# Kernel optimization log

Hardware: AMD Instinct MI355X
Metric: run time of the kernel (lower is better)

The kernel has to match this reference:

```python
import jax
jax.config.update("jax_enable_x64", True)
import jax.numpy as jnp
import numpy as np

SIGMA_2 = 0.1  # SNR = 10 dB -> sigma^2 = 1/10^(10/10)
P = 1.0        # total transmit power

NT, NR, DK, KU, BR = 64, 4, 2, 8, 16
BATCH = 256


def setup_inputs() -> dict:
    key = jax.random.key(0)
    k1, k2 = jax.random.split(key)
    channel = jax.random.normal(k1, (BATCH, NT * NR * BR * 2 * KU), dtype=jnp.float32)
    pred_w = 2 * NR * DK * KU * BR + DK * DK * KU * BR  # 2560
    prediction = jax.random.normal(k2, (BATCH, pred_w), dtype=jnp.float32)
    return {"channel": channel, "prediction": prediction,
            "Nt": NT, "Nr": NR, "dk": DK, "K": KU, "B": BR}


def reference(channel, prediction, Nt, Nr, dk, K, B):
    # --- unpack complex channel: [b, Nt, Nr, B, 2K] -> [b, Nr, Nt, B, K] complex
    Hc = channel.reshape(-1, Nt, Nr, B, 2 * K).astype(jnp.complex128)
    H = Hc[..., :K] + 1j * Hc[..., K:]
    H = jnp.transpose(H, (0, 2, 1, 3, 4))  # [b, Nr, Nt, B, K]

    nu = 2 * Nr * dk * K * B
    u_flat = prediction[:, :nu]
    w_flat = prediction[:, nu:nu + dk * dk * K * B]
    Uc = u_flat.reshape(-1, Nr, dk, B, 2 * K).astype(jnp.complex128)
    U = Uc[..., :K] + 1j * Uc[..., K:]           # [b, Nr, dk, B, K]
    W = w_flat.reshape(-1, dk, dk, B, K).astype(jnp.complex128)  # real-valued W

    # HHU[b,:,:,f,k] = H^H U  -> [b, Nt, dk, B, K]
    HHU = jnp.einsum('brtfk,brdfk->btdfk', jnp.conj(H), U)

    # sum over (rb, user) of sigma2/p * trace(U W U^H)
    tr_UWU = (SIGMA_2 / P) * jnp.einsum('brdfk,bdefk,brefk->b', U, W, jnp.conj(U))
    # sum over (rb, user) of (H^H U) W (H^H U)^H  -> [b, Nt, Nt]
    quad = jnp.einsum('btdfk,bdefk,bsefk->bts', HHU, W, jnp.conj(HHU))
    temp_B = quad + tr_UWU[:, None, None] * jnp.eye(Nt, dtype=jnp.complex128)
    temp_B_inv = jnp.linalg.inv(temp_B)  # batched Nt x Nt complex inverse

    # HUW[b,:,:,k] = sum_rb (H^H U) W  -> [b, Nt, dk, K]
    HUW = jnp.einsum('btdfk,bdefk->btek', HHU, W)
    V0 = jnp.einsum('bts,bsdk->btdk', temp_B_inv, HUW)  # [b, Nt, dk, K]

    # l2-normalize flattened precoder per sample (tf.linalg.normalize)
    flat = V0.reshape(-1, Nt * dk * K)
    flat = flat / jnp.linalg.norm(flat, axis=1, keepdims=True)
    V0 = flat.reshape(-1, Nt, dk, K)

    # power normalization: trace(sum_k V_k V_k^H)
    trace_VV = jnp.einsum('btdk,btdk->b', V0, jnp.conj(V0))
    scale = jnp.sqrt(P / jnp.real(trace_VV).astype(jnp.float32))
    V = V0 * scale.astype(jnp.complex128)[:, None, None, None]

    V = V.reshape(-1, Nt, dk, K, 1)
    return jnp.concatenate([jnp.real(V), jnp.imag(V)], axis=4).astype(jnp.float32)
```

## Files before the change

kernel.cpp:

```cpp
#include <hip/hip_runtime.h>
#include <math.h>


#define SAUG 84
#define STP  65

typedef float v2f __attribute__((ext_vector_type(2)));

namespace {
union alignas(16) ShU {
    struct { float4 TtP[2][2][8][STP]; float4 HtP[2][2][8][STP]; } p1;
    float2 Aug[64][SAUG];
};
union alignas(16) ShV {
    struct { float2 U[4 * 258]; float W[512]; } in;
    float2 xout[64][17];
};
}

__device__ __forceinline__ float2 cmul(float2 x, float2 y) {
    return make_float2(x.x * y.x - x.y * y.y, x.x * y.y + x.y * y.x);
}
__device__ __forceinline__ v2f s2(float s) { return (v2f){s, s}; }

__global__ __launch_bounds__(512, 1)
void uw2v_kernel(const float* __restrict__ channel,
                 const float* __restrict__ prediction,
                 float2* __restrict__ out)
{
    __shared__ ShU sh;
    __shared__ ShV sv;
    __shared__ alignas(16) float2 pivR[2][8][80];
    __shared__ float2 pivI[2][8];
    __shared__ float2 redbuf[8];
    __shared__ float  fred[8];

    const int b   = blockIdx.x;
    const int tid = threadIdx.x;
    const int wv  = tid >> 6;
    const float* pred = prediction + (size_t)b * 2560;
    const float* chan = channel + (size_t)b * 65536;

    #pragma unroll
    for (int i = 0; i < 2; ++i) {
        int m = tid + i * 512;
        int r = m >> 8, d = (m >> 7) & 1, f = (m >> 3) & 15, k = m & 7;
        const float* src = pred + (((r * 2 + d) * 16 + f) << 4);
        sv.in.U[r * 258 + ((d * 16 + f) << 3) + k] = make_float2(src[k], src[k + 8]);
    }
    sv.in.W[tid] = pred[2048 + tid];
    __syncthreads();

    const int half = tid >> 8;
    const int lt   = tid & 255;
    const int t4 = lt >> 2, r4 = lt & 3;
    const int a  = lt >> 4, bb = lt & 15;
    const int bit0 = r4 & 1, bit1 = (r4 >> 1) & 1;
    const int kkb  = 4 * bit0 + 2 * bit1;
    const int mpb  = kkb >> 1;
    const int fbase = half << 3;
    const int tr_r = lt >> 5, tr_d = (lt >> 4) & 1, tr_e = (lt >> 3) & 1, tr_k = lt & 7;

    v2f accA[4][4], accB[4][4];
    #pragma unroll
    for (int i = 0; i < 4; ++i)
        #pragma unroll
        for (int j = 0; j < 4; ++j) {
            accA[i][j] = (v2f){0.f, 0.f};
            accB[i][j] = (v2f){0.f, 0.f};
        }
    float2 huw[4] = {make_float2(0,0), make_float2(0,0), make_float2(0,0), make_float2(0,0)};
    float2 tracc  = make_float2(0.f, 0.f);

    const float* hbase = chan + ((t4 * 4 + r4) << 8) + (fbase << 4);

    #pragma unroll 1
    for (int fi = 0; fi < 8; ++fi) {
        const int f = fbase + fi;
        const float4 ca = *(const float4*)(hbase + (fi << 4) + 0);
        const float4 cb = *(const float4*)(hbase + (fi << 4) + 4);
        const float4 ci = *(const float4*)(hbase + (fi << 4) + 8);
        const float4 cd = *(const float4*)(hbase + (fi << 4) + 12);

        const float4* U0p = (const float4*)&sv.in.U[r4 * 258 + (f << 3)];
        const float4* U1p = (const float4*)&sv.in.U[r4 * 258 + ((16 + f) << 3)];
        const float4 u0q0 = U0p[0], u0q1 = U0p[1], u0q2 = U0p[2], u0q3 = U0p[3];
        const float4 u1q0 = U1p[0], u1q1 = U1p[1], u1q2 = U1p[2], u1q3 = U1p[3];

        float2 val0[8], val1[8];
        #define MK2(K, HR, HI, U0R, U0I, U1R, U1I) \
            val0[K] = make_float2((HR)*(U0R) + (HI)*(U0I), (HR)*(U0I) - (HI)*(U0R)); \
            val1[K] = make_float2((HR)*(U1R) + (HI)*(U1I), (HR)*(U1I) - (HI)*(U1R));
        MK2(0, ca.x, ci.x, u0q0.x, u0q0.y, u1q0.x, u1q0.y)
        MK2(1, ca.y, ci.y, u0q0.z, u0q0.w, u1q0.z, u1q0.w)
        MK2(2, ca.z, ci.z, u0q1.x, u0q1.y, u1q1.x, u1q1.y)
        MK2(3, ca.w, ci.w, u0q1.z, u0q1.w, u1q1.z, u1q1.w)
        MK2(4, cb.x, cd.x, u0q2.x, u0q2.y, u1q2.x, u1q2.y)
        MK2(5, cb.y, cd.y, u0q2.z, u0q2.w, u1q2.z, u1q2.w)
        MK2(6, cb.z, cd.z, u0q3.x, u0q3.y, u1q3.x, u1q3.y)
        MK2(7, cb.w, cd.w, u0q3.z, u0q3.w, u1q3.z, u1q3.w)
        #undef MK2

        float2 s1d0[4], s1d1[4];
        #pragma unroll
        for (int q = 0; q < 4; ++q) {
            float2 k0 = bit0 ? val0[4 + q] : val0[q];
            float2 n0 = bit0 ? val0[q]     : val0[4 + q];
            float2 k1 = bit0 ? val1[4 + q] : val1[q];
            float2 n1 = bit0 ? val1[q]     : val1[4 + q];
            n0.x = __shfl_xor(n0.x, 1); n0.y = __shfl_xor(n0.y, 1);
            n1.x = __shfl_xor(n1.x, 1); n1.y = __shfl_xor(n1.y, 1);
            s1d0[q] = make_float2(k0.x + n0.x, k0.y + n0.y);
            s1d1[q] = make_float2(k1.x + n1.x, k1.y + n1.y);
        }
        float2 h0[2], h1[2];
        #pragma unroll
        for (int jj = 0; jj < 2; ++jj) {
            float2 k0 = bit1 ? s1d0[2 + jj] : s1d0[jj];
            float2 n0 = bit1 ? s1d0[jj]     : s1d0[2 + jj];
            float2 k1 = bit1 ? s1d1[2 + jj] : s1d1[jj];
            float2 n1 = bit1 ? s1d1[jj]     : s1d1[2 + jj];
            n0.x = __shfl_xor(n0.x, 2); n0.y = __shfl_xor(n0.y, 2);
            n1.x = __shfl_xor(n1.x, 2); n1.y = __shfl_xor(n1.y, 2);
            h0[jj] = make_float2(k0.x + n0.x, k0.y + n0.y);
            h1[jj] = make_float2(k1.x + n1.x, k1.y + n1.y);
        }

        if (lt < 128) {
            float w   = sv.in.W[((tr_d * 2 + tr_e) * 16 + f) * 8 + tr_k];
            float2 u1 = sv.in.U[tr_r * 258 + ((tr_d * 16 + f) << 3) + tr_k];
            float2 u2 = sv.in.U[tr_r * 258 + ((tr_e * 16 + f) << 3) + tr_k];
            tracc.x += w * (u1.x * u2.x + u1.y * u2.y);
            tracc.y += w * (u1.y * u2.x - u1.x * u2.y);
        }

        const int p = fi & 1;
        #pragma unroll
        for (int e = 0; e < 2; ++e) {
            float w0a = sv.in.W[(e * 16 + f) * 8 + kkb];
            float w0b = sv.in.W[(e * 16 + f) * 8 + kkb + 1];
            float w1a = sv.in.W[((2 + e) * 16 + f) * 8 + kkb];
            float w1b = sv.in.W[((2 + e) * 16 + f) * 8 + kkb + 1];
            float2 tva = make_float2(h0[0].x * w0a + h1[0].x * w1a,
                                     h0[0].y * w0a + h1[0].y * w1a);
            float2 tvb = make_float2(h0[1].x * w0b + h1[1].x * w1b,
                                     h0[1].y * w0b + h1[1].y * w1b);
            sh.p1.TtP[p][half][e * 4 + mpb][t4] = make_float4(tva.x, tva.y, tvb.x, tvb.y);
            huw[e * 2 + 0].x += tva.x; huw[e * 2 + 0].y += tva.y;
            huw[e * 2 + 1].x += tvb.x; huw[e * 2 + 1].y += tvb.y;
        }
        sh.p1.HtP[p][half][mpb][t4]     = make_float4(h0[0].x, h0[0].y, h0[1].x, h0[1].y);
        sh.p1.HtP[p][half][4 + mpb][t4] = make_float4(h1[0].x, h1[0].y, h1[1].x, h1[1].y);
        __syncthreads();

        #pragma unroll
        for (int mp = 0; mp < 8; ++mp) {
            float4 tq[4], hq[4];
            #pragma unroll
            for (int i = 0; i < 4; ++i) tq[i] = sh.p1.TtP[p][half][mp][a + 16 * i];
            #pragma unroll
            for (int j = 0; j < 4; ++j) hq[j] = sh.p1.HtP[p][half][mp][bb + 16 * j];
            #pragma unroll
            for (int i = 0; i < 4; ++i)
                #pragma unroll
                for (int j = 0; j < 4; ++j) {
                    v2f hq01 = (v2f){hq[j].x, hq[j].y};
                    v2f hq23 = (v2f){hq[j].z, hq[j].w};
                    v2f va = accA[i][j], vb = accB[i][j];
                    va = __builtin_elementwise_fma(s2(tq[i].x), hq01, va);
                    va = __builtin_elementwise_fma(s2(tq[i].z), hq23, va);
                    vb = __builtin_elementwise_fma(s2(tq[i].y), hq01, vb);
                    vb = __builtin_elementwise_fma(s2(tq[i].w), hq23, vb);
                    accA[i][j] = va; accB[i][j] = vb;
                }
        }
    }

    #pragma unroll
    for (int off = 32; off; off >>= 1) {
        tracc.x += __shfl_xor(tracc.x, off);
        tracc.y += __shfl_xor(tracc.y, off);
    }
    if ((tid & 63) == 0) redbuf[wv] = tracc;
    __syncthreads();
    float2 trv = make_float2(0.f, 0.f);
    #pragma unroll
    for (int w = 0; w < 8; ++w) { trv.x += redbuf[w].x; trv.y += redbuf[w].y; }
    trv.x *= 0.1f; trv.y *= 0.1f;

    if (half == 0) {
        #pragma unroll
        for (int i = 0; i < 4; ++i)
            #pragma unroll
            for (int j = 0; j < 4; ++j) {
                float2 v = make_float2(accA[i][j].x + accB[i][j].y,
                                       accB[i][j].x - accA[i][j].y);
                int row = a + 16 * i, col = bb + 16 * j;
                if (row == col) { v.x += trv.x; v.y += trv.y; }
                sh.Aug[row][col] = v;
            }
        #pragma unroll
        for (int e = 0; e < 2; ++e)
            #pragma unroll
            for (int jj = 0; jj < 2; ++jj)
                sh.Aug[t4][64 + e * 8 + kkb + jj] = huw[e * 2 + jj];
    }
    __syncthreads();
    if (half == 1) {
        #pragma unroll
        for (int i = 0; i < 4; ++i)
            #pragma unroll
            for (int j = 0; j < 4; ++j) {
                int row = a + 16 * i, col = bb + 16 * j;
                float2 v = sh.Aug[row][col];
                v.x += accA[i][j].x + accB[i][j].y;
                v.y += accB[i][j].x - accA[i][j].y;
                sh.Aug[row][col] = v;
            }
        #pragma unroll
        for (int e = 0; e < 2; ++e)
            #pragma unroll
            for (int jj = 0; jj < 2; ++jj) {
                int col = 64 + e * 8 + kkb + jj;
                float2 v = sh.Aug[t4][col];
                v.x += huw[e * 2 + jj].x; v.y += huw[e * 2 + jj].y;
                sh.Aug[t4][col] = v;
            }
    }
    __syncthreads();

    const int gi = tid >> 3, gc = tid & 7;
    const int cb = 10 * gc;
    const int lanebase = (tid & 63) & 56;

    v2f xr[10];
    {
        const float4* rp = (const float4*)&sh.Aug[gi][cb];
        float4 q0 = rp[0], q1 = rp[1], q2 = rp[2], q3 = rp[3], q4 = rp[4];
        xr[0] = (v2f){q0.x, q0.y}; xr[1] = (v2f){q0.z, q0.w};
        xr[2] = (v2f){q1.x, q1.y}; xr[3] = (v2f){q1.z, q1.w};
        xr[4] = (v2f){q2.x, q2.y}; xr[5] = (v2f){q2.z, q2.w};
        xr[6] = (v2f){q3.x, q3.y}; xr[7] = (v2f){q3.z, q3.w};
        xr[8] = (v2f){q4.x, q4.y}; xr[9] = (v2f){q4.z, q4.w};
    }

    float2 myipv = make_float2(0.f, 0.f);

    auto rowupd = [](v2f* xr10, const v2f* pr10, float2 L) {
        v2f nLx = s2(-L.x);
        v2f Lyp = (v2f){L.y, -L.y};
        #pragma unroll
        for (int c = 0; c < 10; ++c) {
            v2f prv = pr10[c];
            v2f prsw = (v2f){prv.y, prv.x};
            xr10[c] = __builtin_elementwise_fma(
                nLx, prv, __builtin_elementwise_fma(Lyp, prsw, xr10[c]));
        }
    };

    auto cascade = [&](int chunk, int nb) {
        #pragma unroll
        for (int p = 0; p < 8; ++p) {
            const int col = 8 * chunk + p;
            const int cs  = col / 10;
            float2 cand = make_float2(0.f, 0.f);
            #pragma unroll
            for (int c = 0; c < 10; ++c)
                if (cb + c == col) cand = make_float2(xr[c].x, xr[c].y);
            float2 z, Lv;
            z.x  = __shfl(cand.x, p * 8 + cs);
            z.y  = __shfl(cand.y, p * 8 + cs);
            Lv.x = __shfl(cand.x, lanebase + cs);
            Lv.y = __shfl(cand.y, lanebase + cs);
            float  zi  = 1.0f / (z.x * z.x + z.y * z.y);
            float2 ipv = make_float2(z.x * zi, -z.y * zi);
            const bool isPiv = (gi == col);
            if (isPiv) myipv = ipv;
            v2f pr[10];
            #pragma unroll
            for (int c = 0; c < 10; ++c) {
                pr[c].x = __shfl(xr[c].x, p * 8 + gc);
                pr[c].y = __shfl(xr[c].y, p * 8 + gc);
            }
            if (!isPiv) {
                float2 L = cmul(Lv, ipv);
                rowupd(xr, pr, L);
            }
        }
        const int prw = gi & 7;
        float4* wp = (float4*)&pivR[nb][prw][cb];
        wp[0] = make_float4(xr[0].x, xr[0].y, xr[1].x, xr[1].y);
        wp[1] = make_float4(xr[2].x, xr[2].y, xr[3].x, xr[3].y);
        wp[2] = make_float4(xr[4].x, xr[4].y, xr[5].x, xr[5].y);
        wp[3] = make_float4(xr[6].x, xr[6].y, xr[7].x, xr[7].y);
        wp[4] = make_float4(xr[8].x, xr[8].y, xr[9].x, xr[9].y);
        if (gc == 0) pivI[nb][prw] = myipv;
    };

    auto eliminate = [&](int chunk, int bf) {
        #pragma unroll
        for (int p = 0; p < 8; ++p) {
            const int col = 8 * chunk + p;
            float2 cand = make_float2(0.f, 0.f);
            #pragma unroll
            for (int c = 0; c < 10; ++c)
                if (cb + c == col) cand = make_float2(xr[c].x, xr[c].y);
            float2 Lv;
            Lv.x = __shfl(cand.x, lanebase + col / 10);
            Lv.y = __shfl(cand.y, lanebase + col / 10);
            float2 ipv = pivI[bf][p];
            float2 L = cmul(Lv, ipv);
            const float4* pp = (const float4*)&pivR[bf][p][cb];
            float4 p0 = pp[0], p1 = pp[1], p2 = pp[2], p3 = pp[3], p4 = pp[4];
            v2f pr[10];
            pr[0] = (v2f){p0.x, p0.y}; pr[1] = (v2f){p0.z, p0.w};
            pr[2] = (v2f){p1.x, p1.y}; pr[3] = (v2f){p1.z, p1.w};
            pr[4] = (v2f){p2.x, p2.y}; pr[5] = (v2f){p2.z, p2.w};
            pr[6] = (v2f){p3.x, p3.y}; pr[7] = (v2f){p3.z, p3.w};
            pr[8] = (v2f){p4.x, p4.y}; pr[9] = (v2f){p4.z, p4.w};
            rowupd(xr, pr, L);
        }
    };

    int cur = 0;
    if (wv == 0) cascade(0, 0);
    __syncthreads();

    #pragma unroll 1
    for (int c = 0; c < 8; ++c) {
        if (wv != c) {
            eliminate(c, cur);
            if (wv == c + 1) cascade(c + 1, cur ^ 1);
        }
        __syncthreads();
        cur ^= 1;
    }

    float ss = 0.f;
    if (gc == 6) {
        #pragma unroll
        for (int c = 4; c < 10; ++c) {
            float2 xv = cmul(make_float2(xr[c].x, xr[c].y), myipv);
            ss += xv.x * xv.x + xv.y * xv.y;
            sv.xout[gi][c - 4] = xv;
        }
    } else if (gc == 7) {
        #pragma unroll
        for (int c = 0; c < 10; ++c) {
            float2 xv = cmul(make_float2(xr[c].x, xr[c].y), myipv);
            ss += xv.x * xv.x + xv.y * xv.y;
            sv.xout[gi][6 + c] = xv;
        }
    }
    #pragma unroll
    for (int off = 32; off; off >>= 1) ss += __shfl_xor(ss, off);
    if ((tid & 63) == 0) fred[wv] = ss;
    __syncthreads();
    float total = 0.f;
    #pragma unroll
    for (int w = 0; w < 8; ++w) total += fred[w];
    float invn = rsqrtf(total);
    #pragma unroll
    for (int q = 0; q < 2; ++q) {
        int m = tid + q * 512;
        float2 v = sv.xout[m >> 4][m & 15];
        out[(size_t)b * 1024 + m] = make_float2(v.x * invn, v.y * invn);
    }
}

extern "C" void kernel_launch(void* const* d_in, const int* in_sizes, int n_in,
                              void* d_out, int out_size, void* d_ws, size_t ws_size,
                              hipStream_t stream) {
    const float* channel    = (const float*)d_in[0];
    const float* prediction = (const float*)d_in[1];
    int batch = in_sizes[0] / 65536;
    uw2v_kernel<<<dim3(batch), dim3(512), 0, stream>>>(channel, prediction,
                                                       (float2*)d_out);
}
```

Baseline: 155.0 us.

## Partition H^H U work by user pairs instead of receive antennas, removing shuffles

Each lane of a quad now owns two users (k pairs) and loops over all four receive antennas itself, instead of owning one antenna and reducing across lanes with two rounds of xor shuffles. Channel loads become float2 reads from four rows rather than four float4 reads of one row, and U/W loads become vectorized per user pair. This removes the cross-lane shuffle reduction and the wasted products, at the cost of narrower, more scattered global loads.

```diff
diff --git a/kernel.cpp b/kernel.cpp
--- a/kernel.cpp
+++ b/kernel.cpp
@@ -53,11 +53,9 @@
 
     const int half = tid >> 8;
     const int lt   = tid & 255;
-    const int t4 = lt >> 2, r4 = lt & 3;
+    const int t4 = lt >> 2, kq = lt & 3;
     const int a  = lt >> 4, bb = lt & 15;
-    const int bit0 = r4 & 1, bit1 = (r4 >> 1) & 1;
-    const int kkb  = 4 * bit0 + 2 * bit1;
-    const int mpb  = kkb >> 1;
+    const int kk0 = 2 * kq;
     const int fbase = half << 3;
     const int tr_r = lt >> 5, tr_d = (lt >> 4) & 1, tr_e = (lt >> 3) & 1, tr_k = lt & 7;
 
@@ -72,58 +70,33 @@
     float2 huw[4] = {make_float2(0,0), make_float2(0,0), make_float2(0,0), make_float2(0,0)};
     float2 tracc  = make_float2(0.f, 0.f);
 
-    const float* hbase = chan + ((t4 * 4 + r4) << 8) + (fbase << 4);
+    const float* chanT = chan + ((t4 * 4) << 8) + (fbase << 4);
 
     #pragma unroll 1
     for (int fi = 0; fi < 8; ++fi) {
         const int f = fbase + fi;
-        const float4 ca = *(const float4*)(hbase + (fi << 4) + 0);
-        const float4 cb = *(const float4*)(hbase + (fi << 4) + 4);
-        const float4 ci = *(const float4*)(hbase + (fi << 4) + 8);
-        const float4 cd = *(const float4*)(hbase + (fi << 4) + 12);
-
-        const float4* U0p = (const float4*)&sv.in.U[r4 * 258 + (f << 3)];
-        const float4* U1p = (const float4*)&sv.in.U[r4 * 258 + ((16 + f) << 3)];
-        const float4 u0q0 = U0p[0], u0q1 = U0p[1], u0q2 = U0p[2], u0q3 = U0p[3];
-        const float4 u1q0 = U1p[0], u1q1 = U1p[1], u1q2 = U1p[2], u1q3 = U1p[3];
-
-        float2 val0[8], val1[8];
-        #define MK2(K, HR, HI, U0R, U0I, U1R, U1I) \
-            val0[K] = make_float2((HR)*(U0R) + (HI)*(U0I), (HR)*(U0I) - (HI)*(U0R)); \
-            val1[K] = make_float2((HR)*(U1R) + (HI)*(U1I), (HR)*(U1I) - (HI)*(U1R));
-        MK2(0, ca.x, ci.x, u0q0.x, u0q0.y, u1q0.x, u1q0.y)
-        MK2(1, ca.y, ci.y, u0q0.z, u0q0.w, u1q0.z, u1q0.w)
-        MK2(2, ca.z, ci.z, u0q1.x, u0q1.y, u1q1.x, u1q1.y)
-        MK2(3, ca.w, ci.w, u0q1.z, u0q1.w, u1q1.z, u1q1.w)
-        MK2(4, cb.x, cd.x, u0q2.x, u0q2.y, u1q2.x, u1q2.y)
-        MK2(5, cb.y, cd.y, u0q2.z, u0q2.w, u1q2.z, u1q2.w)
-        MK2(6, cb.z, cd.z, u0q3.x, u0q3.y, u1q3.x, u1q3.y)
-        MK2(7, cb.w, cd.w, u0q3.z, u0q3.w, u1q3.z, u1q3.w)
-        #undef MK2
-
-        float2 s1d0[4], s1d1[4];
-        #pragma unroll
-        for (int q = 0; q < 4; ++q) {
-            float2 k0 = bit0 ? val0[4 + q] : val0[q];
-            float2 n0 = bit0 ? val0[q]     : val0[4 + q];
-            float2 k1 = bit0 ? val1[4 + q] : val1[q];
-            float2 n1 = bit0 ? val1[q]     : val1[4 + q];
-            n0.x = __shfl_xor(n0.x, 1); n0.y = __shfl_xor(n0.y, 1);
-            n1.x = __shfl_xor(n1.x, 1); n1.y = __shfl_xor(n1.y, 1);
-            s1d0[q] = make_float2(k0.x + n0.x, k0.y + n0.y);
-            s1d1[q] = make_float2(k1.x + n1.x, k1.y + n1.y);
-        }
-        float2 h0[2], h1[2];
-        #pragma unroll
-        for (int jj = 0; jj < 2; ++jj) {
-            float2 k0 = bit1 ? s1d0[2 + jj] : s1d0[jj];
-            float2 n0 = bit1 ? s1d0[jj]     : s1d0[2 + jj];
-            float2 k1 = bit1 ? s1d1[2 + jj] : s1d1[jj];
-            float2 n1 = bit1 ? s1d1[jj]     : s1d1[2 + jj];
-            n0.x = __shfl_xor(n0.x, 2); n0.y = __shfl_xor(n0.y, 2);
-            n1.x = __shfl_xor(n1.x, 2); n1.y = __shfl_xor(n1.y, 2);
-            h0[jj] = make_float2(k0.x + n0.x, k0.y + n0.y);
-            h1[jj] = make_float2(k1.x + n1.x, k1.y + n1.y);
+
+        const float* cb0 = chanT + (fi << 4);
+        float2 hre[4], him[4];
+        #pragma unroll
+        for (int r = 0; r < 4; ++r) {
+            const float* rp = cb0 + (r << 8);
+            hre[r] = *(const float2*)(rp + kk0);
+            him[r] = *(const float2*)(rp + 8 + kk0);
+        }
+
+        float2 hh[2][2] = {{make_float2(0,0), make_float2(0,0)},
+                           {make_float2(0,0), make_float2(0,0)}};
+        #pragma unroll
+        for (int r = 0; r < 4; ++r) {
+            #pragma unroll
+            for (int d = 0; d < 2; ++d) {
+                const float4 u = *(const float4*)&sv.in.U[r * 258 + ((d * 16 + f) << 3) + kk0];
+                hh[d][0].x += hre[r].x * u.x + him[r].x * u.y;
+                hh[d][0].y += hre[r].x * u.y - him[r].x * u.x;
+                hh[d][1].x += hre[r].y * u.z + him[r].y * u.w;
+                hh[d][1].y += hre[r].y * u.w - him[r].y * u.z;
+            }
         }
 
         if (lt < 128) {
@@ -137,20 +110,18 @@
         const int p = fi & 1;
         #pragma unroll
         for (int e = 0; e < 2; ++e) {
-            float w0a = sv.in.W[(e * 16 + f) * 8 + kkb];
-            float w0b = sv.in.W[(e * 16 + f) * 8 + kkb + 1];
-            float w1a = sv.in.W[((2 + e) * 16 + f) * 8 + kkb];
-            float w1b = sv.in.W[((2 + e) * 16 + f) * 8 + kkb + 1];
-            float2 tva = make_float2(h0[0].x * w0a + h1[0].x * w1a,
-                                     h0[0].y * w0a + h1[0].y * w1a);
-            float2 tvb = make_float2(h0[1].x * w0b + h1[1].x * w1b,
-                                     h0[1].y * w0b + h1[1].y * w1b);
-            sh.p1.TtP[p][half][e * 4 + mpb][t4] = make_float4(tva.x, tva.y, tvb.x, tvb.y);
+            const float2 w0 = *(const float2*)&sv.in.W[(e * 16 + f) * 8 + kk0];
+            const float2 w1 = *(const float2*)&sv.in.W[((2 + e) * 16 + f) * 8 + kk0];
+            float2 tva = make_float2(hh[0][0].x * w0.x + hh[1][0].x * w1.x,
+                                     hh[0][0].y * w0.x + hh[1][0].y * w1.x);
+            float2 tvb = make_float2(hh[0][1].x * w0.y + hh[1][1].x * w1.y,
+                                     hh[0][1].y * w0.y + hh[1][1].y * w1.y);
+            sh.p1.TtP[p][half][e * 4 + kq][t4] = make_float4(tva.x, tva.y, tvb.x, tvb.y);
             huw[e * 2 + 0].x += tva.x; huw[e * 2 + 0].y += tva.y;
             huw[e * 2 + 1].x += tvb.x; huw[e * 2 + 1].y += tvb.y;
         }
-        sh.p1.HtP[p][half][mpb][t4]     = make_float4(h0[0].x, h0[0].y, h0[1].x, h0[1].y);
-        sh.p1.HtP[p][half][4 + mpb][t4] = make_float4(h1[0].x, h1[0].y, h1[1].x, h1[1].y);
+        sh.p1.HtP[p][half][kq][t4]     = make_float4(hh[0][0].x, hh[0][0].y, hh[0][1].x, hh[0][1].y);
+        sh.p1.HtP[p][half][4 + kq][t4] = make_float4(hh[1][0].x, hh[1][0].y, hh[1][1].x, hh[1][1].y);
         __syncthreads();
 
         #pragma unroll
@@ -203,7 +174,7 @@
         for (int e = 0; e < 2; ++e)
             #pragma unroll
             for (int jj = 0; jj < 2; ++jj)
-                sh.Aug[t4][64 + e * 8 + kkb + jj] = huw[e * 2 + jj];
+                sh.Aug[t4][64 + e * 8 + kk0 + jj] = huw[e * 2 + jj];
     }
     __syncthreads();
     if (half == 1) {
@@ -221,7 +192,7 @@
         for (int e = 0; e < 2; ++e)
             #pragma unroll
             for (int jj = 0; jj < 2; ++jj) {
-                int col = 64 + e * 8 + kkb + jj;
+                int col = 64 + e * 8 + kk0 + jj;
                 float2 v = sh.Aug[t4][col];
                 v.x += huw[e * 2 + jj].x; v.y += huw[e * 2 + jj].y;
                 sh.Aug[t4][col] = v;
```

Measured after the change: 151.9 us. 1.02x faster.
